# Optimization experiments

Hardware: AMD Instinct MI355X
Metric: run time of the kernel (lower is better)

Reference implementation:

```python
import jax, jax.numpy as jnp
import numpy as np

EPS = 1e-12  # F.normalize default eps


def _l2_normalize(x, axis):
    n = jnp.sqrt(jnp.sum(x * x, axis=axis, keepdims=True))
    return x / jnp.maximum(n, EPS)


def setup_inputs() -> dict:
    key = jax.random.key(0)
    k1, k2 = jax.random.split(key)
    code = jax.random.normal(k1, (8, 768, 32, 32), dtype=jnp.float32)
    clusters = jax.random.normal(k2, (64, 768), dtype=jnp.float32)
    return {"code": code, "clusters": clusters, "image_hw": 512}


def reference(code, clusters, image_hw):
    # L2-normalize cluster centroids over channel dim and features over C
    normed_clusters = _l2_normalize(clusters, axis=1)            # [N, C]
    normed_features = _l2_normalize(code, axis=1)                # [B, C, H, W]
    # cosine similarity to every cluster
    inner_products = jnp.einsum('bchw,nc->bnhw', normed_features, normed_clusters)  # [B,N,H,W]
    # hard nearest-cluster assignment -> one-hot over N (channel axis 1)
    assign = jnp.argmax(inner_products, axis=1)                  # [B, H, W] int
    n_classes = clusters.shape[0]
    cluster_probs = jnp.moveaxis(
        jax.nn.one_hot(assign, n_classes, dtype=jnp.float32), -1, 1)  # [B,N,H,W]
    # training loss: negative mean of selected (max) similarity
    cluster_loss = -jnp.mean(jnp.sum(cluster_probs * inner_products, axis=1))
    # resize_to(cluster_probs, image): bilinear upsample to image resolution
    B, N = cluster_probs.shape[0], cluster_probs.shape[1]
    resized = jax.image.resize(cluster_probs, (B, N, image_hw, image_hw), method='bilinear')
    return (cluster_loss, resized, code)
```

## Files before the change

### kernel.cpp

```cpp
#include <hip/hip_runtime.h>

#define CCH 768
#define NCL 64
#define HWIN 1024
#define RES_ELEMS 134217728LL
#define CODE_ELEMS 6291456LL
#define ZQUADS 33554431LL
#define CQUADS 1572863LL
#define WUNITS (ZQUADS + CQUADS)
#define PREP_ZBLOCKS 137216

__global__ __launch_bounds__(256) void k_prep(const float* __restrict__ clusters,
                                              const float* __restrict__ code,
                                              float* __restrict__ nc_t,
                                              float* __restrict__ out)
{
    int tid = threadIdx.x;
    int blk = blockIdx.x;
    if (blk < NCL) {
        __shared__ float red[256];
        int n = blk;
        float v0 = clusters[n * CCH + tid];
        float v1 = clusters[n * CCH + tid + 256];
        float v2 = clusters[n * CCH + tid + 512];
        red[tid] = v0 * v0 + v1 * v1 + v2 * v2;
        __syncthreads();
        for (int off = 128; off > 0; off >>= 1) {
            if (tid < off) red[tid] += red[tid + off];
            __syncthreads();
        }
        float scale = 1.0f / fmaxf(sqrtf(red[0]), 1e-12f);
        nc_t[(tid      ) * NCL + n] = v0 * scale;
        nc_t[(tid + 256) * NCL + n] = v1 * scale;
        nc_t[(tid + 512) * NCL + n] = v2 * scale;
        if (n == 0 && tid == 0) out[0] = 0.0f;
        return;
    }
    long long u = (long long)(blk - NCL) * 256 + tid;
    if (u < ZQUADS) {
        *(float4*)(out + 4 + 4 * u) = make_float4(0.f, 0.f, 0.f, 0.f);
        if (u == 0) {
            out[1] = 0.f; out[2] = 0.f; out[3] = 0.f;
            out[RES_ELEMS] = 0.f;
            out[RES_ELEMS + 1] = code[0];
            out[RES_ELEMS + 2] = code[1];
            out[RES_ELEMS + 3] = code[2];
            out[1 + RES_ELEMS + CODE_ELEMS - 1] = code[CODE_ELEMS - 1];
        }
    } else if (u < WUNITS) {
        long long c = u - ZQUADS;
        const float* src = code + 3 + 4 * c;
        float4 v = make_float4(src[0], src[1], src[2], src[3]);
        *(float4*)(out + (RES_ELEMS + 4) + 4 * c) = v;
    }
}

__global__ __launch_bounds__(256) void k_assign(const float* __restrict__ code,
                                                const float* __restrict__ nc_t,
                                                int* __restrict__ assign,
                                                float* __restrict__ out)
{
    __shared__ float lds_nc[64 * 64];
    __shared__ float lds_red[8 * 2048];
    __shared__ float lds_sq[8 * 32];

    int tid = threadIdx.x;
    int blk = blockIdx.x;
    int cg = tid >> 5;
    int ng = (tid >> 3) & 3;
    int pg = tid & 7;
    int b = blk >> 5;
    int pixb = (blk & 31) << 5;
    const float* codeB = code + (size_t)b * CCH * HWIN + pixb + (pg << 2);

    float acc[4][16];
    #pragma unroll
    for (int p = 0; p < 4; ++p) {
        #pragma unroll
        for (int q = 0; q < 16; ++q) acc[p][q] = 0.f;
    }
    float sq0 = 0.f, sq1 = 0.f, sq2 = 0.f, sq3 = 0.f;

    for (int k = 0; k < 12; ++k) {
        __syncthreads();
        const float4* src = (const float4*)(nc_t + k * 4096);
        float4* dst = (float4*)lds_nc;
        #pragma unroll
        for (int i = 0; i < 4; ++i) dst[tid + 256 * i] = src[tid + 256 * i];
        __syncthreads();
        #pragma unroll
        for (int m = 0; m < 8; ++m) {
            int ch = k * 64 + cg * 8 + m;
            float4 f = *(const float4*)(codeB + ch * HWIN);
            sq0 += f.x * f.x; sq1 += f.y * f.y; sq2 += f.z * f.z; sq3 += f.w * f.w;
            const float* ncrow = lds_nc + ((cg * 8 + m) << 6) + (ng << 4);
            #pragma unroll
            for (int q = 0; q < 16; ++q) {
                float w = ncrow[q];
                acc[0][q] += f.x * w;
                acc[1][q] += f.y * w;
                acc[2][q] += f.z * w;
                acc[3][q] += f.w * w;
            }
        }
    }

    #pragma unroll
    for (int p = 0; p < 4; ++p) {
        float4* dstp = (float4*)&lds_red[cg * 2048 + (pg * 4 + p) * 64 + ng * 16];
        dstp[0] = make_float4(acc[p][0],  acc[p][1],  acc[p][2],  acc[p][3]);
        dstp[1] = make_float4(acc[p][4],  acc[p][5],  acc[p][6],  acc[p][7]);
        dstp[2] = make_float4(acc[p][8],  acc[p][9],  acc[p][10], acc[p][11]);
        dstp[3] = make_float4(acc[p][12], acc[p][13], acc[p][14], acc[p][15]);
    }
    if (ng == 0) {
        lds_sq[cg * 32 + pg * 4 + 0] = sq0;
        lds_sq[cg * 32 + pg * 4 + 1] = sq1;
        lds_sq[cg * 32 + pg * 4 + 2] = sq2;
        lds_sq[cg * 32 + pg * 4 + 3] = sq3;
    }
    __syncthreads();

    for (int idx = tid; idx < 2048; idx += 256) {
        float s = 0.f;
        #pragma unroll
        for (int c2 = 0; c2 < 8; ++c2) s += lds_red[c2 * 2048 + idx];
        lds_nc[idx] = s;
    }
    __syncthreads();

    if (tid < 32) {
        float ss = 0.f;
        #pragma unroll
        for (int c2 = 0; c2 < 8; ++c2) ss += lds_sq[c2 * 32 + tid];
        float inv = 1.0f / fmaxf(sqrtf(ss), 1e-12f);
        float best = -1e30f; int bi = 0;
        for (int n = 0; n < 64; ++n) {
            float v = lds_nc[tid * 64 + n];
            if (v > best) { best = v; bi = n; }
        }
        assign[blk * 32 + tid] = bi;
        float l = best * inv;
        l += __shfl_down(l, 16);
        l += __shfl_down(l, 8);
        l += __shfl_down(l, 4);
        l += __shfl_down(l, 2);
        l += __shfl_down(l, 1);
        if (tid == 0) atomicAdd(out, -l * (1.0f / 8192.0f));
    }
}

__global__ __launch_bounds__(256) void k_sparse(const int* __restrict__ assign,
                                                float* __restrict__ out)
{
    int tid = threadIdx.x;
    int row = blockIdx.x * 2 + (tid >> 7);
    int t = tid & 127;
    int b = row >> 9;
    int i = row & 511;
    const int* ab = assign + (b << 10);

    float xi = (i + 0.5f) * 0.0625f - 0.5f;
    float fif = floorf(xi);
    int ii = (int)fif;
    float fi = xi - fif;
    int i0 = ii < 0 ? 0 : ii;
    int i1 = (ii + 1) > 31 ? 31 : (ii + 1);
    const int* r0 = ab + (i0 << 5);
    const int* r1 = ab + (i1 << 5);
    float* base = out + 1 + ((long long)b << 24) + ((long long)i << 9);

    auto emit = [&](int j) {
        float xj = (j + 0.5f) * 0.0625f - 0.5f;
        float fjf = floorf(xj);
        int jj = (int)fjf;
        float fj = xj - fjf;
        int j0 = jj < 0 ? 0 : jj;
        int j1 = (jj + 1) > 31 ? 31 : (jj + 1);
        int   ids[4] = { r0[j0], r0[j1], r1[j0], r1[j1] };
        float ws[4]  = { (1.f - fi) * (1.f - fj), (1.f - fi) * fj,
                         fi * (1.f - fj),         fi * fj };
        bool dead[4] = { false, false, false, false };
        #pragma unroll
        for (int k2 = 1; k2 < 4; ++k2) {
            #pragma unroll
            for (int m = 0; m < k2; ++m) {
                if (!dead[k2] && !dead[m] && ids[k2] == ids[m]) {
                    ws[m] += ws[k2];
                    dead[k2] = true;
                }
            }
        }
        #pragma unroll
        for (int k2 = 0; k2 < 4; ++k2) {
            if (!dead[k2]) base[((long long)ids[k2] << 18) + j] = ws[k2];
        }
    };

    if (t == 0) { emit(0); emit(1); emit(2); emit(511); }
    else { int jb = 4 * t - 1; emit(jb); emit(jb + 1); emit(jb + 2); emit(jb + 3); }
}

extern "C" void kernel_launch(void* const* d_in, const int* in_sizes, int n_in,
                              void* d_out, int out_size, void* d_ws, size_t ws_size,
                              hipStream_t stream)
{
    const float* code     = (const float*)d_in[0];
    const float* clusters = (const float*)d_in[1];
    float* out = (float*)d_out;
    float* nc_t = (float*)d_ws;
    int* assign = (int*)((char*)d_ws + 196608);

    k_prep  <<<64 + PREP_ZBLOCKS, 256, 0, stream>>>(clusters, code, nc_t, out);
    k_assign<<<256,               256, 0, stream>>>(code, nc_t, assign, out);
    k_sparse<<<2048,              256, 0, stream>>>(assign, out);
}
```

Baseline: 662.8 us.

## Replace zero-fill plus sparse scatter with dense one-pass resize writes

```diff
diff --git a/kernel.cpp b/kernel.cpp
--- a/kernel.cpp
+++ b/kernel.cpp
@@ -5,53 +5,37 @@
 #define HWIN 1024
 #define RES_ELEMS 134217728LL
 #define CODE_ELEMS 6291456LL
-#define ZQUADS 33554431LL
 #define CQUADS 1572863LL
-#define WUNITS (ZQUADS + CQUADS)
-#define PREP_ZBLOCKS 137216
-
-__global__ __launch_bounds__(256) void k_prep(const float* __restrict__ clusters,
+#define COPY_BLOCKS 1536
+#define DENSE_BLOCKS 4096
+
+__global__ __launch_bounds__(256) void k_norm(const float* __restrict__ clusters,
                                               const float* __restrict__ code,
                                               float* __restrict__ nc_t,
                                               float* __restrict__ out)
 {
     int tid = threadIdx.x;
-    int blk = blockIdx.x;
-    if (blk < NCL) {
-        __shared__ float red[256];
-        int n = blk;
-        float v0 = clusters[n * CCH + tid];
-        float v1 = clusters[n * CCH + tid + 256];
-        float v2 = clusters[n * CCH + tid + 512];
-        red[tid] = v0 * v0 + v1 * v1 + v2 * v2;
+    int n = blockIdx.x;
+    __shared__ float red[256];
+    float v0 = clusters[n * CCH + tid];
+    float v1 = clusters[n * CCH + tid + 256];
+    float v2 = clusters[n * CCH + tid + 512];
+    red[tid] = v0 * v0 + v1 * v1 + v2 * v2;
+    __syncthreads();
+    for (int off = 128; off > 0; off >>= 1) {
+        if (tid < off) red[tid] += red[tid + off];
         __syncthreads();
-        for (int off = 128; off > 0; off >>= 1) {
-            if (tid < off) red[tid] += red[tid + off];
-            __syncthreads();
-        }
-        float scale = 1.0f / fmaxf(sqrtf(red[0]), 1e-12f);
-        nc_t[(tid      ) * NCL + n] = v0 * scale;
-        nc_t[(tid + 256) * NCL + n] = v1 * scale;
-        nc_t[(tid + 512) * NCL + n] = v2 * scale;
-        if (n == 0 && tid == 0) out[0] = 0.0f;
-        return;
-    }
-    long long u = (long long)(blk - NCL) * 256 + tid;
-    if (u < ZQUADS) {
-        *(float4*)(out + 4 + 4 * u) = make_float4(0.f, 0.f, 0.f, 0.f);
-        if (u == 0) {
-            out[1] = 0.f; out[2] = 0.f; out[3] = 0.f;
-            out[RES_ELEMS] = 0.f;
-            out[RES_ELEMS + 1] = code[0];
-            out[RES_ELEMS + 2] = code[1];
-            out[RES_ELEMS + 3] = code[2];
-            out[1 + RES_ELEMS + CODE_ELEMS - 1] = code[CODE_ELEMS - 1];
-        }
-    } else if (u < WUNITS) {
-        long long c = u - ZQUADS;
-        const float* src = code + 3 + 4 * c;
-        float4 v = make_float4(src[0], src[1], src[2], src[3]);
-        *(float4*)(out + (RES_ELEMS + 4) + 4 * c) = v;
+    }
+    float scale = 1.0f / fmaxf(sqrtf(red[0]), 1e-12f);
+    nc_t[(tid      ) * NCL + n] = v0 * scale;
+    nc_t[(tid + 256) * NCL + n] = v1 * scale;
+    nc_t[(tid + 512) * NCL + n] = v2 * scale;
+    if (n == 0 && tid == 0) {
+        out[0] = 0.0f;
+        out[RES_ELEMS + 1] = code[0];
+        out[RES_ELEMS + 2] = code[1];
+        out[RES_ELEMS + 3] = code[2];
+        out[RES_ELEMS + CODE_ELEMS] = code[CODE_ELEMS - 1];
     }
 }
 
@@ -75,10 +59,9 @@
 
     float acc[4][16];
     #pragma unroll
-    for (int p = 0; p < 4; ++p) {
+    for (int p = 0; p < 4; ++p)
         #pragma unroll
         for (int q = 0; q < 16; ++q) acc[p][q] = 0.f;
-    }
     float sq0 = 0.f, sq1 = 0.f, sq2 = 0.f, sq3 = 0.f;
 
     for (int k = 0; k < 12; ++k) {
@@ -150,15 +133,32 @@
     }
 }
 
-__global__ __launch_bounds__(256) void k_sparse(const int* __restrict__ assign,
-                                                float* __restrict__ out)
+__global__ __launch_bounds__(256) void k_dense(const int* __restrict__ assign,
+                                               const float* __restrict__ code,
+                                               float* __restrict__ out)
 {
     int tid = threadIdx.x;
-    int row = blockIdx.x * 2 + (tid >> 7);
-    int t = tid & 127;
-    int b = row >> 9;
-    int i = row & 511;
-    const int* ab = assign + (b << 10);
+    int blk = blockIdx.x;
+
+    if (blk >= DENSE_BLOCKS) {
+        long long u = (long long)(blk - DENSE_BLOCKS) * 256 + tid;
+        #pragma unroll
+        for (int k = 0; k < 4; ++k) {
+            long long q = u + (long long)k * (COPY_BLOCKS * 256);
+            if (q < CQUADS) {
+                const float* src = code + 3 + 4 * q;
+                float4 v = make_float4(src[0], src[1], src[2], src[3]);
+                *(float4*)(out + RES_ELEMS + 4 + 4 * q) = v;
+            }
+        }
+        return;
+    }
+
+    int b = blk >> 9;
+    int i = blk & 511;
+    __shared__ int   s_r0[32], s_r1[32];
+    __shared__ int4  s_ids[128];
+    __shared__ float4 s_fj[128];
 
     float xi = (i + 0.5f) * 0.0625f - 0.5f;
     float fif = floorf(xi);
@@ -166,39 +166,67 @@
     float fi = xi - fif;
     int i0 = ii < 0 ? 0 : ii;
     int i1 = (ii + 1) > 31 ? 31 : (ii + 1);
-    const int* r0 = ab + (i0 << 5);
-    const int* r1 = ab + (i1 << 5);
-    float* base = out + 1 + ((long long)b << 24) + ((long long)i << 9);
-
-    auto emit = [&](int j) {
-        float xj = (j + 0.5f) * 0.0625f - 0.5f;
-        float fjf = floorf(xj);
-        int jj = (int)fjf;
-        float fj = xj - fjf;
-        int j0 = jj < 0 ? 0 : jj;
-        int j1 = (jj + 1) > 31 ? 31 : (jj + 1);
-        int   ids[4] = { r0[j0], r0[j1], r1[j0], r1[j1] };
-        float ws[4]  = { (1.f - fi) * (1.f - fj), (1.f - fi) * fj,
-                         fi * (1.f - fj),         fi * fj };
-        bool dead[4] = { false, false, false, false };
-        #pragma unroll
-        for (int k2 = 1; k2 < 4; ++k2) {
-            #pragma unroll
-            for (int m = 0; m < k2; ++m) {
-                if (!dead[k2] && !dead[m] && ids[k2] == ids[m]) {
-                    ws[m] += ws[k2];
-                    dead[k2] = true;
-                }
-            }
-        }
-        #pragma unroll
-        for (int k2 = 0; k2 < 4; ++k2) {
-            if (!dead[k2]) base[((long long)ids[k2] << 18) + j] = ws[k2];
-        }
-    };
-
-    if (t == 0) { emit(0); emit(1); emit(2); emit(511); }
-    else { int jb = 4 * t - 1; emit(jb); emit(jb + 1); emit(jb + 2); emit(jb + 3); }
+
+    if (tid < 32) {
+        s_r0[tid] = assign[(b << 10) + (i0 << 5) + tid];
+        s_r1[tid] = assign[(b << 10) + (i1 << 5) + tid];
+    }
+    __syncthreads();
+
+    if (tid < 128) {
+        int s = tid;
+        int4 ids; float4 fj4;
+        int jl[4];
+        if (s == 0) { jl[0] = 0; jl[1] = 1; jl[2] = 2; jl[3] = 511; }
+        else { jl[0] = 4 * s - 1; jl[1] = 4 * s; jl[2] = 4 * s + 1; jl[3] = 4 * s + 2; }
+        int pk[4]; float fjv[4];
+        #pragma unroll
+        for (int k = 0; k < 4; ++k) {
+            int j = jl[k];
+            float xj = (j + 0.5f) * 0.0625f - 0.5f;
+            float fjf = floorf(xj);
+            int jj = (int)fjf;
+            fjv[k] = xj - fjf;
+            int j0 = jj < 0 ? 0 : jj;
+            int j1 = (jj + 1) > 31 ? 31 : (jj + 1);
+            pk[k] = s_r0[j0] | (s_r0[j1] << 8) | (s_r1[j0] << 16) | (s_r1[j1] << 24);
+        }
+        ids.x = pk[0]; ids.y = pk[1]; ids.z = pk[2]; ids.w = pk[3];
+        fj4.x = fjv[0]; fj4.y = fjv[1]; fj4.z = fjv[2]; fj4.w = fjv[3];
+        s_ids[s] = ids;
+        s_fj[s] = fj4;
+    }
+    __syncthreads();
+
+    float fi1 = 1.0f - fi;
+    long long rowoff = 1LL + ((long long)b << 24) + ((long long)i << 9);
+
+    #pragma unroll 4
+    for (int it = 0; it < 32; ++it) {
+        int task = it * 256 + tid;
+        int n = task >> 7;
+        int s = task & 127;
+        int4 p4 = s_ids[s];
+        float4 f4 = s_fj[s];
+        float v[4];
+        int pks[4] = { p4.x, p4.y, p4.z, p4.w };
+        float fjs[4] = { f4.x, f4.y, f4.z, f4.w };
+        #pragma unroll
+        for (int k = 0; k < 4; ++k) {
+            int p = pks[k];
+            float P = (((p      ) & 255) == n ? fi1 : 0.f)
+                    + (((p >> 16) & 255) == n ? fi  : 0.f);
+            float Q = (((p >>  8) & 255) == n ? fi1 : 0.f)
+                    + (((p >> 24) & 255) == n ? fi  : 0.f);
+            v[k] = P + fjs[k] * (Q - P);
+        }
+        float* rowbase = out + rowoff + ((long long)n << 18);
+        if (s == 0) {
+            rowbase[0] = v[0]; rowbase[1] = v[1]; rowbase[2] = v[2]; rowbase[511] = v[3];
+        } else {
+            *(float4*)(rowbase + 4 * s - 1) = make_float4(v[0], v[1], v[2], v[3]);
+        }
+    }
 }
 
 extern "C" void kernel_launch(void* const* d_in, const int* in_sizes, int n_in,
@@ -211,7 +239,7 @@
     float* nc_t = (float*)d_ws;
     int* assign = (int*)((char*)d_ws + 196608);
 
-    k_prep  <<<64 + PREP_ZBLOCKS, 256, 0, stream>>>(clusters, code, nc_t, out);
-    k_assign<<<256,               256, 0, stream>>>(code, nc_t, assign, out);
-    k_sparse<<<2048,              256, 0, stream>>>(assign, out);
-}
+    k_norm  <<<NCL,                       256, 0, stream>>>(clusters, code, nc_t, out);
+    k_assign<<<256,                       256, 0, stream>>>(code, nc_t, assign, out);
+    k_dense <<<DENSE_BLOCKS + COPY_BLOCKS, 256, 0, stream>>>(assign, code, out);
+}
```

After: 640.3 us. -3.4%, faster.
